# Kernel tuning notes

Hardware: AMD Instinct MI355X
Metric: run time of the kernel (lower is better)

The kernel has to match this reference:

```python
import jax, jax.numpy as jnp
import numpy as np

BN_EPS = 1e-5


def setup_inputs() -> dict:
    key = jax.random.key(0)
    ks = jax.random.split(key, 12)
    N, K, C_IN, C_OUT = 50000, 16, 128, 128
    C2 = 2 * C_OUT
    return {
        "features": jax.random.normal(ks[0], (N, C_IN), dtype=jnp.float32),
        "neighbor_idx": jax.random.randint(ks[1], (N, K), 0, N, dtype=jnp.int64),
        "W1": jax.random.normal(ks[2], (C_IN, C2), dtype=jnp.float32) * 0.05,
        "b1": jax.random.normal(ks[3], (C2,), dtype=jnp.float32) * 0.05,
        "gamma": jax.random.uniform(ks[4], (C2,), dtype=jnp.float32, minval=0.5, maxval=1.5),
        "beta": jax.random.normal(ks[5], (C2,), dtype=jnp.float32) * 0.05,
        "run_mean": jax.random.normal(ks[6], (C2,), dtype=jnp.float32) * 0.05,
        "run_var": jax.random.uniform(ks[7], (C2,), dtype=jnp.float32, minval=0.5, maxval=1.5),
        "Ws": jax.random.normal(ks[8], (C2, C2), dtype=jnp.float32) * 0.05,
        "Wm": jax.random.normal(ks[9], (C2, C_OUT), dtype=jnp.float32) * 0.05,
        "bm": jax.random.normal(ks[10], (C_OUT,), dtype=jnp.float32) * 0.05,
    }


def reference(features, neighbor_idx, W1, b1, gamma, beta, run_mean, run_var, Ws, Wm, bm):
    # mlp1: Linear + ReLU (no BN)
    x = jax.nn.relu(features @ W1 + b1)                     # (N, 2C)
    # gather_neighbour: irregular index_select
    g = x[neighbor_idx]                                     # (N, k, 2C)
    # BatchNorm1d over channel dim (inference semantics, running stats)
    inv = gamma * jax.lax.rsqrt(run_var + BN_EPS)
    g = (g - run_mean) * inv + beta                         # (N, k, 2C)
    # AttentivePooling: per-neighbor score linear (no bias), softmax over k
    scores = jax.nn.softmax(g @ Ws, axis=1)                 # (N, k, 2C)
    feat = jnp.sum(scores * g, axis=1)                      # (N, 2C)
    return feat @ Wm + bm                                   # (N, C_out)
```

## Files before the change

### kernel.cpp

```cpp
#include <hip/hip_runtime.h>
#include <cstddef>

#define C_IN  128
#define C2    256
#define C_OUT 128
#define KNBR  16
#define PTS   32

typedef unsigned short u16;
typedef __attribute__((ext_vector_type(8))) short bf16x8;
typedef __attribute__((ext_vector_type(8))) unsigned short u16x8;
typedef __attribute__((ext_vector_type(4))) float f32x4;

__device__ __forceinline__ float bf2f(u16 h) {
    return __uint_as_float(((unsigned int)h) << 16);
}
__device__ __forceinline__ u16 f2bf(float x) {
    unsigned int u = __float_as_uint(x);
    return (u16)((u + 0x7fffu + ((u >> 16) & 1u)) >> 16);
}

__global__ void prep_k(const float* __restrict__ W1, const float* __restrict__ Ws,
                       const float* __restrict__ Wm, u16* __restrict__ W1t,
                       u16* __restrict__ Wst, u16* __restrict__ Wmt)
{
    const int n = blockIdx.x, t = threadIdx.x;
    if (blockIdx.y == 0) {
        if (t < 128) W1t[n * 128 + t] = f2bf(W1[t * 256 + n]);
    } else if (blockIdx.y == 1) {
        Wst[n * 256 + t] = f2bf(Ws[t * 256 + n]);
    } else {
        if (n < 128) Wmt[n * 256 + t] = f2bf(Wm[t * 128 + n]);
    }
}


__global__ __launch_bounds__(256)
void mlp_k(const float* __restrict__ F, const u16* __restrict__ W1t,
           const u16* __restrict__ Wst,
           const float* __restrict__ bias, const float* __restrict__ gamma,
           const float* __restrict__ beta, const float* __restrict__ mean,
           const float* __restrict__ var,
           u16* __restrict__ packed, int N)
{
    __shared__ u16 As[64][136];
    __shared__ u16 Bs[128][72];
    __shared__ u16 xs[64][264];

    const int tid = threadIdx.x;
    const int w = tid >> 6, l = tid & 63, q = l >> 4, r = l & 15;
    const int wm = w & 1, wn = w >> 1;
    const int m0 = blockIdx.x * 64;

    #pragma unroll
    for (int i = 0; i < 8; i++) {
        int idx = tid + i * 256;
        int row = idx >> 5, c4 = (idx & 31) * 4;
        int gm = m0 + row;
        float4 v = make_float4(0.f, 0.f, 0.f, 0.f);
        if (gm < N) v = *(const float4*)(F + (size_t)gm * C_IN + c4);
        ushort4 h;
        h.x = f2bf(v.x); h.y = f2bf(v.y); h.z = f2bf(v.z); h.w = f2bf(v.w);
        *(ushort4*)&As[row][c4] = h;
    }

    #pragma unroll
    for (int nh = 0; nh < 2; nh++) {
        f32x4 acc[2][4] = {};
        #pragma unroll 1
        for (int k0 = 0; k0 < C_IN; k0 += 64) {
            __syncthreads();
            #pragma unroll
            for (int i = 0; i < 4; i++) {
                int idx = tid + i * 256;
                int row = idx >> 3, g = (idx & 7) * 8;
                *(uint4*)&Bs[row][g] = *(const uint4*)(
                    W1t + (size_t)(nh * 128 + row) * C_IN + k0 + g);
            }
            __syncthreads();
            #pragma unroll
            for (int h = 0; h < 2; h++) {
                bf16x8 af[2], bfr[4];
                #pragma unroll
                for (int i = 0; i < 2; i++)
                    af[i] = *(const bf16x8*)&As[wm * 32 + i * 16 + r][k0 + h * 32 + q * 8];
                #pragma unroll
                for (int j = 0; j < 4; j++)
                    bfr[j] = *(const bf16x8*)&Bs[wn * 64 + j * 16 + r][h * 32 + q * 8];
                #pragma unroll
                for (int i = 0; i < 2; i++)
                    #pragma unroll
                    for (int j = 0; j < 4; j++)
                        acc[i][j] = __builtin_amdgcn_mfma_f32_16x16x32_bf16(
                            af[i], bfr[j], acc[i][j], 0, 0, 0);
            }
        }
        #pragma unroll
        for (int j = 0; j < 4; j++) {
            const int ch = nh * 128 + wn * 64 + j * 16 + r;
            const float bi = bias[ch], be = beta[ch], mu = mean[ch];
            const float iv = gamma[ch] * rsqrtf(var[ch] + 1e-5f);
            #pragma unroll
            for (int i = 0; i < 2; i++) {
                const int mb = wm * 32 + i * 16 + q * 4;
                #pragma unroll
                for (int p = 0; p < 4; p++) {
                    float x = fmaxf(acc[i][j][p] + bi, 0.f);
                    x = (x - mu) * iv + be;
                    xs[mb + p][ch] = f2bf(x);
                }
            }
        }
    }
    __syncthreads();

    #pragma unroll
    for (int nh = 0; nh < 2; nh++) {
        f32x4 acc[2][4] = {};
        #pragma unroll 1
        for (int k0 = 0; k0 < C2; k0 += 64) {
            __syncthreads();
            #pragma unroll
            for (int i = 0; i < 4; i++) {
                int idx = tid + i * 256;
                int row = idx >> 3, g = (idx & 7) * 8;
                *(uint4*)&Bs[row][g] = *(const uint4*)(
                    Wst + (size_t)(nh * 128 + row) * C2 + k0 + g);
            }
            __syncthreads();
            #pragma unroll
            for (int h = 0; h < 2; h++) {
                bf16x8 af[2], bfr[4];
                #pragma unroll
                for (int i = 0; i < 2; i++)
                    af[i] = *(const bf16x8*)&xs[wm * 32 + i * 16 + r][k0 + h * 32 + q * 8];
                #pragma unroll
                for (int j = 0; j < 4; j++)
                    bfr[j] = *(const bf16x8*)&Bs[wn * 64 + j * 16 + r][h * 32 + q * 8];
                #pragma unroll
                for (int i = 0; i < 2; i++)
                    #pragma unroll
                    for (int j = 0; j < 4; j++)
                        acc[i][j] = __builtin_amdgcn_mfma_f32_16x16x32_bf16(
                            af[i], bfr[j], acc[i][j], 0, 0, 0);
            }
        }
        __syncthreads();
        #pragma unroll
        for (int j = 0; j < 4; j++) {
            const int chl = wn * 64 + j * 16 + r;
            #pragma unroll
            for (int i = 0; i < 2; i++) {
                const int mb = wm * 32 + i * 16 + q * 4;
                #pragma unroll
                for (int p = 0; p < 4; p++)
                    As[mb + p][chl] = f2bf(__expf(acc[i][j][p]));
            }
        }
        __syncthreads();
        #pragma unroll
        for (int i = 0; i < 8; i++) {
            int idx = tid + i * 256;
            int row = idx >> 5, slot = idx & 31;
            int c0 = slot * 4;
            if (m0 + row < N) {
                ushort4 e  = *(const ushort4*)&As[row][c0];
                ushort4 xv = *(const ushort4*)&xs[row][nh * 128 + c0];
                uint4 qv;
                qv.x = (unsigned)e.x | ((unsigned)xv.x << 16);
                qv.y = (unsigned)e.y | ((unsigned)xv.y << 16);
                qv.z = (unsigned)e.z | ((unsigned)xv.z << 16);
                qv.w = (unsigned)e.w | ((unsigned)xv.w << 16);
                *(uint4*)(packed + (size_t)(m0 + row) * 512 + nh * 256 + slot * 8) = qv;
            }
        }
    }
}

__global__ __launch_bounds__(256)
void gather_out_k(const u16* __restrict__ packed, const int* __restrict__ nidx,
                  const u16* __restrict__ Bt, const float* __restrict__ bias,
                  float* __restrict__ Cf, int N)
{
    __shared__ int rows[PTS * KNBR];
    __shared__ u16 Bs[128][72];
    __shared__ __align__(16) u16 fsm[PTS * 264];

    const int tid = threadIdx.x;
    const int w = tid >> 6, l = tid & 63, q = l >> 4, r = l & 15;
    const int m0 = blockIdx.x * PTS;

    #pragma unroll
    for (int i = 0; i < 2; i++) {
        int idx = tid + i * 256;
        int n = m0 + (idx >> 4);
        rows[idx] = (n < N) ? nidx[n * KNBR + (idx & 15)] : 0;
    }
    __syncthreads();

    #pragma unroll 1
    for (int ip = 0; ip < 8; ip++) {
        const int pl = w * 8 + ip;
        u16x8 v[KNBR];
        #pragma unroll
        for (int k = 0; k < KNBR; k++)
            v[k] = *(const u16x8*)(packed + (size_t)rows[pl * KNBR + k] * 512 + l * 8);
        float num[4] = {0.f, 0.f, 0.f, 0.f};
        float den[4] = {0.f, 0.f, 0.f, 0.f};
        #pragma unroll
        for (int k = 0; k < KNBR; k++) {
            #pragma unroll
            for (int c = 0; c < 4; c++) {
                float e = bf2f((u16)v[k][2 * c]);
                float x = bf2f((u16)v[k][2 * c + 1]);
                den[c] += e;
                num[c] = fmaf(e, x, num[c]);
            }
        }
        ushort4 o;
        o.x = f2bf(num[0] / den[0]); o.y = f2bf(num[1] / den[1]);
        o.z = f2bf(num[2] / den[2]); o.w = f2bf(num[3] / den[3]);
        *(ushort4*)&fsm[pl * 264 + l * 4] = o;
    }
    __syncthreads();

    const int wm = w & 1, wn = w >> 1;
    f32x4 acc[4] = {};

    #pragma unroll 1
    for (int k0 = 0; k0 < C2; k0 += 64) {
        __syncthreads();
        #pragma unroll
        for (int i = 0; i < 4; i++) {
            int idx = tid + i * 256;
            int row = idx >> 3, g = (idx & 7) * 8;
            *(uint4*)&Bs[row][g] = *(const uint4*)(
                Bt + (size_t)row * C2 + k0 + g);
        }
        __syncthreads();
        #pragma unroll
        for (int h = 0; h < 2; h++) {
            bf16x8 af, bfr[4];
            af = *(const bf16x8*)&fsm[(wm * 16 + r) * 264 + k0 + h * 32 + q * 8];
            #pragma unroll
            for (int j = 0; j < 4; j++)
                bfr[j] = *(const bf16x8*)&Bs[wn * 64 + j * 16 + r][h * 32 + q * 8];
            #pragma unroll
            for (int j = 0; j < 4; j++)
                acc[j] = __builtin_amdgcn_mfma_f32_16x16x32_bf16(
                    af, bfr[j], acc[j], 0, 0, 0);
        }
    }
    __syncthreads();

    float* STF = (float*)fsm;
    #pragma unroll
    for (int j = 0; j < 4; j++) {
        const int ch = wn * 64 + j * 16 + r;
        const float bo = bias[ch];
        const int mb = wm * 16 + q * 4;
        #pragma unroll
        for (int p = 0; p < 4; p++)
            STF[(mb + p) * 132 + ch] = acc[j][p] + bo;
    }
    __syncthreads();
    #pragma unroll
    for (int i = 0; i < 4; i++) {
        int idx = tid + i * 256;
        int row = idx >> 5, c4 = (idx & 31) * 4;
        if (m0 + row < N)
            *(float4*)(Cf + (size_t)(m0 + row) * C_OUT + c4) =
                *(const float4*)&STF[row * 132 + c4];
    }
}

extern "C" void kernel_launch(void* const* d_in, const int* in_sizes, int n_in,
                              void* d_out, int out_size, void* d_ws, size_t ws_size,
                              hipStream_t stream)
{
    const float* features = (const float*)d_in[0];
    const int*   nidx     = (const int*)d_in[1];
    const float* W1       = (const float*)d_in[2];
    const float* b1       = (const float*)d_in[3];
    const float* gamma    = (const float*)d_in[4];
    const float* beta     = (const float*)d_in[5];
    const float* mean     = (const float*)d_in[6];
    const float* var      = (const float*)d_in[7];
    const float* Ws       = (const float*)d_in[8];
    const float* Wm       = (const float*)d_in[9];
    const float* bm       = (const float*)d_in[10];
    float* out = (float*)d_out;

    const int N = in_sizes[0] / C_IN;

    u16* packed = (u16*)d_ws;
    u16* W1t    = packed + (size_t)N * 512;
    u16* Wst    = W1t + 256 * 128;
    u16* Wmt    = Wst + 256 * 256;

    prep_k<<<dim3(256, 3), 256, 0, stream>>>(W1, Ws, Wm, W1t, Wst, Wmt);

    const int MT = (N + 63) / 64;
    const int GT = (N + PTS - 1) / PTS;

    mlp_k<<<MT, 256, 0, stream>>>(features, W1t, Wst, b1, gamma, beta,
                                  mean, var, packed, N);
    gather_out_k<<<GT, 256, 0, stream>>>(packed, nidx, Wmt, bm, out, N);
}
```

Before: 255.0 us.

## Precompute BN params, store packed directly, read Wm from global in gather

Folds bias, BN scale and shift into a precomputed float4 table built in the prep kernel. Keeps the normalized activations in registers and writes exp/activation pairs straight to global, dropping the LDS staging pass and several barriers. The gather kernel loads neighbours in two halves to lower register pressure, sets a minimum occupancy hint, and reads Wm fragments from global instead of staging them through LDS. The cost is narrower, less coalesced global stores and uncached-in-LDS weight reads.

```diff
diff --git a/kernel.cpp b/kernel.cpp
--- a/kernel.cpp
+++ b/kernel.cpp
@@ -21,26 +21,29 @@
 }
 
 __global__ void prep_k(const float* __restrict__ W1, const float* __restrict__ Ws,
-                       const float* __restrict__ Wm, u16* __restrict__ W1t,
-                       u16* __restrict__ Wst, u16* __restrict__ Wmt)
+                       const float* __restrict__ Wm, const float* __restrict__ b1,
+                       const float* __restrict__ gamma, const float* __restrict__ beta,
+                       const float* __restrict__ mean, const float* __restrict__ var,
+                       u16* __restrict__ W1t, u16* __restrict__ Wst,
+                       u16* __restrict__ Wmt, float4* __restrict__ bnp)
 {
     const int n = blockIdx.x, t = threadIdx.x;
     if (blockIdx.y == 0) {
         if (t < 128) W1t[n * 128 + t] = f2bf(W1[t * 256 + n]);
     } else if (blockIdx.y == 1) {
         Wst[n * 256 + t] = f2bf(Ws[t * 256 + n]);
-    } else {
+    } else if (blockIdx.y == 2) {
         if (n < 128) Wmt[n * 256 + t] = f2bf(Wm[t * 128 + n]);
+    } else if (n == 0) {
+        float iv = gamma[t] * rsqrtf(var[t] + 1e-5f);
+        bnp[t] = make_float4(b1[t], iv, beta[t] - mean[t] * iv, 0.f);
     }
 }
 
 
 __global__ __launch_bounds__(256)
 void mlp_k(const float* __restrict__ F, const u16* __restrict__ W1t,
-           const u16* __restrict__ Wst,
-           const float* __restrict__ bias, const float* __restrict__ gamma,
-           const float* __restrict__ beta, const float* __restrict__ mean,
-           const float* __restrict__ var,
+           const u16* __restrict__ Wst, const float4* __restrict__ bnp,
            u16* __restrict__ packed, int N)
 {
     __shared__ u16 As[64][136];
@@ -64,6 +67,8 @@
         *(ushort4*)&As[row][c4] = h;
     }
 
+    ushort4 xr[2][2][4];
+
     #pragma unroll
     for (int nh = 0; nh < 2; nh++) {
         f32x4 acc[2][4] = {};
@@ -98,21 +103,23 @@
         #pragma unroll
         for (int j = 0; j < 4; j++) {
             const int ch = nh * 128 + wn * 64 + j * 16 + r;
-            const float bi = bias[ch], be = beta[ch], mu = mean[ch];
-            const float iv = gamma[ch] * rsqrtf(var[ch] + 1e-5f);
+            const float4 bp = bnp[ch];
             #pragma unroll
             for (int i = 0; i < 2; i++) {
                 const int mb = wm * 32 + i * 16 + q * 4;
+                ushort4 hx;
                 #pragma unroll
                 for (int p = 0; p < 4; p++) {
-                    float x = fmaxf(acc[i][j][p] + bi, 0.f);
-                    x = (x - mu) * iv + be;
-                    xs[mb + p][ch] = f2bf(x);
+                    float x = fmaxf(acc[i][j][p] + bp.x, 0.f) * bp.y + bp.z;
+                    u16 h = f2bf(x);
+                    xs[mb + p][ch] = h;
+                    if (p == 0) hx.x = h; else if (p == 1) hx.y = h;
+                    else if (p == 2) hx.z = h; else hx.w = h;
                 }
-            }
-        }
-    }
-    __syncthreads();
+                xr[nh][i][j] = hx;
+            }
+        }
+    }
 
     #pragma unroll
     for (int nh = 0; nh < 2; nh++) {
@@ -145,45 +152,35 @@
                             af[i], bfr[j], acc[i][j], 0, 0, 0);
             }
         }
-        __syncthreads();
         #pragma unroll
         for (int j = 0; j < 4; j++) {
-            const int chl = wn * 64 + j * 16 + r;
+            const int ch = nh * 128 + wn * 64 + j * 16 + r;
             #pragma unroll
             for (int i = 0; i < 2; i++) {
                 const int mb = wm * 32 + i * 16 + q * 4;
-                #pragma unroll
-                for (int p = 0; p < 4; p++)
-                    As[mb + p][chl] = f2bf(__expf(acc[i][j][p]));
-            }
-        }
-        __syncthreads();
-        #pragma unroll
-        for (int i = 0; i < 8; i++) {
-            int idx = tid + i * 256;
-            int row = idx >> 5, slot = idx & 31;
-            int c0 = slot * 4;
-            if (m0 + row < N) {
-                ushort4 e  = *(const ushort4*)&As[row][c0];
-                ushort4 xv = *(const ushort4*)&xs[row][nh * 128 + c0];
-                uint4 qv;
-                qv.x = (unsigned)e.x | ((unsigned)xv.x << 16);
-                qv.y = (unsigned)e.y | ((unsigned)xv.y << 16);
-                qv.z = (unsigned)e.z | ((unsigned)xv.z << 16);
-                qv.w = (unsigned)e.w | ((unsigned)xv.w << 16);
-                *(uint4*)(packed + (size_t)(m0 + row) * 512 + nh * 256 + slot * 8) = qv;
-            }
-        }
-    }
-}
-
-__global__ __launch_bounds__(256)
+                const ushort4 hx = xr[nh][i][j];
+                #pragma unroll
+                for (int p = 0; p < 4; p++) {
+                    const int gm = m0 + mb + p;
+                    if (gm < N) {
+                        unsigned xv = (p == 0) ? hx.x : (p == 1) ? hx.y
+                                    : (p == 2) ? hx.z : hx.w;
+                        unsigned ey = f2bf(__expf(acc[i][j][p]));
+                        *(unsigned*)(packed + (size_t)gm * 512 + ch * 2) =
+                            ey | (xv << 16);
+                    }
+                }
+            }
+        }
+    }
+}
+
+__global__ __launch_bounds__(256, 5)
 void gather_out_k(const u16* __restrict__ packed, const int* __restrict__ nidx,
                   const u16* __restrict__ Bt, const float* __restrict__ bias,
                   float* __restrict__ Cf, int N)
 {
     __shared__ int rows[PTS * KNBR];
-    __shared__ u16 Bs[128][72];
     __shared__ __align__(16) u16 fsm[PTS * 264];
 
     const int tid = threadIdx.x;
@@ -201,20 +198,24 @@
     #pragma unroll 1
     for (int ip = 0; ip < 8; ip++) {
         const int pl = w * 8 + ip;
-        u16x8 v[KNBR];
-        #pragma unroll
-        for (int k = 0; k < KNBR; k++)
-            v[k] = *(const u16x8*)(packed + (size_t)rows[pl * KNBR + k] * 512 + l * 8);
         float num[4] = {0.f, 0.f, 0.f, 0.f};
         float den[4] = {0.f, 0.f, 0.f, 0.f};
-        #pragma unroll
-        for (int k = 0; k < KNBR; k++) {
-            #pragma unroll
-            for (int c = 0; c < 4; c++) {
-                float e = bf2f((u16)v[k][2 * c]);
-                float x = bf2f((u16)v[k][2 * c + 1]);
-                den[c] += e;
-                num[c] = fmaf(e, x, num[c]);
+        #pragma unroll 1
+        for (int hf = 0; hf < 2; hf++) {
+            u16x8 v[8];
+            #pragma unroll
+            for (int k = 0; k < 8; k++)
+                v[k] = *(const u16x8*)(packed +
+                    (size_t)rows[pl * KNBR + hf * 8 + k] * 512 + l * 8);
+            #pragma unroll
+            for (int k = 0; k < 8; k++) {
+                #pragma unroll
+                for (int c = 0; c < 4; c++) {
+                    float e = bf2f((u16)v[k][2 * c]);
+                    float x = bf2f((u16)v[k][2 * c + 1]);
+                    den[c] += e;
+                    num[c] = fmaf(e, x, num[c]);
+                }
             }
         }
         ushort4 o;
@@ -227,24 +228,16 @@
     const int wm = w & 1, wn = w >> 1;
     f32x4 acc[4] = {};
 
-    #pragma unroll 1
+    #pragma unroll
     for (int k0 = 0; k0 < C2; k0 += 64) {
-        __syncthreads();
-        #pragma unroll
-        for (int i = 0; i < 4; i++) {
-            int idx = tid + i * 256;
-            int row = idx >> 3, g = (idx & 7) * 8;
-            *(uint4*)&Bs[row][g] = *(const uint4*)(
-                Bt + (size_t)row * C2 + k0 + g);
-        }
-        __syncthreads();
         #pragma unroll
         for (int h = 0; h < 2; h++) {
             bf16x8 af, bfr[4];
             af = *(const bf16x8*)&fsm[(wm * 16 + r) * 264 + k0 + h * 32 + q * 8];
             #pragma unroll
             for (int j = 0; j < 4; j++)
-                bfr[j] = *(const bf16x8*)&Bs[wn * 64 + j * 16 + r][h * 32 + q * 8];
+                bfr[j] = *(const bf16x8*)(Bt +
+                    (size_t)(wn * 64 + j * 16 + r) * C2 + k0 + h * 32 + q * 8);
             #pragma unroll
             for (int j = 0; j < 4; j++)
                 acc[j] = __builtin_amdgcn_mfma_f32_16x16x32_bf16(
@@ -297,13 +290,14 @@
     u16* W1t    = packed + (size_t)N * 512;
     u16* Wst    = W1t + 256 * 128;
     u16* Wmt    = Wst + 256 * 256;
-
-    prep_k<<<dim3(256, 3), 256, 0, stream>>>(W1, Ws, Wm, W1t, Wst, Wmt);
+    float4* bnp = (float4*)(Wmt + 128 * 256);
+
+    prep_k<<<dim3(256, 4), 256, 0, stream>>>(W1, Ws, Wm, b1, gamma, beta,
+                                             mean, var, W1t, Wst, Wmt, bnp);
 
     const int MT = (N + 63) / 64;
     const int GT = (N + PTS - 1) / PTS;
 
-    mlp_k<<<MT, 256, 0, stream>>>(features, W1t, Wst, b1, gamma, beta,
-                                  mean, var, packed, N);
+    mlp_k<<<MT, 256, 0, stream>>>(features, W1t, Wst, bnp, packed, N);
     gather_out_k<<<GT, 256, 0, stream>>>(packed, nidx, Wmt, bm, out, N);
 }
```

Result: faster. 244.0 us (median of 2 runs) (-4.3%).
